# Performance work log

Measured on AMD Instinct MI355X. Metric: run time of the kernel, lower is better.

Reference implementation:

```python
import jax, jax.numpy as jnp
from jax import lax
import numpy as np

B, C, T = 4096, 22, 1001   # batch, EEG channels, time samples
K, KSZ, P = 40, 25, 100    # num_kernels, kernel_size, pool_size
S, O = 9, 4                # num_subjects, n_outputs
FEAT = K * ((T - KSZ + 1) // P)  # 40*9 = 360
BN_EPS = 1e-5


def setup_inputs() -> dict:
    key = jax.random.key(0)
    ks = jax.random.split(key, 8)
    x = jax.random.normal(ks[0], (B, C, T + 1), dtype=jnp.float32)
    # subject ids in 1..S encoded as id*1e6 in the last time step (all channels; only ch 0 is read)
    ids = jax.random.randint(ks[1], (B,), 1, S + 1)
    x = x.at[:, :, -1].set((ids * 1000000).astype(jnp.float32)[:, None])
    conv_w = jax.random.normal(ks[2], (K, C, 1, KSZ), dtype=jnp.float32) * 0.05
    conv_b = jax.random.normal(ks[3], (K,), dtype=jnp.float32) * 0.05
    bn_gamma = jnp.ones((K,), dtype=jnp.float32)
    bn_beta = jnp.zeros((K,), dtype=jnp.float32)
    fc_w = jax.random.normal(ks[4], (S, FEAT, O), dtype=jnp.float32) * 0.05
    fc_b = jax.random.normal(ks[5], (S, O), dtype=jnp.float32) * 0.05
    return {"x": x, "conv_w": conv_w, "conv_b": conv_b,
            "bn_gamma": bn_gamma, "bn_beta": bn_beta,
            "fc_w": fc_w, "fc_b": fc_b}


def reference(x, conv_w, conv_b, bn_gamma, bn_beta, fc_w, fc_b):
    # subject index (0-based); int cast blocks gradient flow, matching .item() dispatch
    sid = jnp.round(x[:, 0, -1] / 1e6).astype(jnp.int32) - 1  # [B]
    xin = x[:, :, :-1][:, :, None, :]                          # [B, C, 1, T]
    # Conv2d(n_chans, num_kernels, (1, kernel_size)), VALID padding
    y = lax.conv_general_dilated(xin, conv_w, window_strides=(1, 1),
                                 padding='VALID',
                                 dimension_numbers=('NCHW', 'OIHW', 'NCHW'))
    y = y + conv_b[None, :, None, None]                        # [B, K, 1, W], W = T-KSZ+1
    y = jax.nn.elu(y)
    # BatchNorm2d with batch statistics (train mode), affine
    mean = jnp.mean(y, axis=(0, 2, 3), keepdims=True)
    var = jnp.var(y, axis=(0, 2, 3), keepdims=True)
    y = (y - mean) * lax.rsqrt(var + BN_EPS)
    y = y * bn_gamma[None, :, None, None] + bn_beta[None, :, None, None]
    # AvgPool2d((1, P)): non-overlapping windows, remainder dropped
    W = y.shape[-1]
    n = W // P
    y = y[:, :, 0, :n * P].reshape(B, K, n, P).mean(axis=-1)   # [B, K, n]
    feat = y.reshape(B, -1)                                     # [B, FEAT]
    # dropout is identity at inference
    # per-sample subject-indexed FC, vectorized as a gathered batched matvec
    out = jnp.einsum('bf,bfo->bo', feat, fc_w[sid]) + fc_b[sid]  # [B, O]
    return out
```

## Files before the change

kernel.cpp:

```cpp
#include <hip/hip_runtime.h>

#define BATCH 4096
#define CCH   22
#define TT    1001
#define TROW  1002
#define KOUT  40
#define KSZ   25
#define WOUT  977
#define POOLW 100
#define NWIN  9
#define FEAT  360
#define NOUT  4

#define WBLK  256
#define NWB   4
#define NBLK  (BATCH * NWB)
#define CSTG  24
#define ROWB  48
#define TSTG  288
#define FKK   19
#define KP    48
#define NLOC  4

typedef __attribute__((ext_vector_type(8))) short short8;
typedef __attribute__((ext_vector_type(4))) float floatx4;

__device__ __forceinline__ unsigned short f2bf(float f) {
    unsigned u = __float_as_uint(f);
    u += 0x7fff + ((u >> 16) & 1);
    return (unsigned short)(u >> 16);
}
__device__ __forceinline__ unsigned cvt_pk_bf16(float a, float b) {
    unsigned r;
    asm("v_cvt_pk_bf16_f32 %0, %1, %2" : "=v"(r) : "v"(a), "v"(b));
    return r;
}
__device__ __forceinline__ float eluf(float v) {
    return v > 0.0f ? v : __expf(v) - 1.0f;
}

__global__ __launch_bounds__(256) void pack_w_kernel(const float* __restrict__ cw,
                                                     unsigned short* __restrict__ wp) {
    int i = blockIdx.x * 256 + threadIdx.x;
    if (i >= FKK * KP * 32) return;
    int e = i & 31;
    int n = (i >> 5) % KP;
    int kk = i / (KP * 32);
    int f = kk * 32 + e;
    int j = f / CSTG, c = f - j * CSTG;
    float v = (n < KOUT && c < CCH && j < KSZ) ? cw[(n * CCH + c) * KSZ + j] : 0.0f;
    wp[i] = f2bf(v);
}

__global__ __launch_bounds__(256, 4) void conv_mfma_kernel(
        const float* __restrict__ x, const unsigned short* __restrict__ wp,
        const float* __restrict__ cb, float* __restrict__ pparts,
        float* __restrict__ spS, float* __restrict__ spQ) {
    __shared__ unsigned short xt[TSTG * CSTG];
    __shared__ float ps_s[NLOC * KP];
    __shared__ float st_q[KP];

    const int bx = blockIdx.x, b = blockIdx.y;
    const int w0   = (bx == 0) ? 0   : (bx == 1 ? 252 : (bx == 2 ? 500 : 752));
    const int oend = (bx == 0) ? 252 : (bx == 1 ? 500 : (bx == 2 ? 752 : WOUT));
    const int tid = threadIdx.x;
    const int wv = __builtin_amdgcn_readfirstlane(tid >> 6);
    const int lane = tid & 63;
    const size_t xb = (size_t)b * (CCH * TROW);

    for (int i = tid; i < NLOC * KP + KP; i += 256) {
        if (i < NLOC * KP) ps_s[i] = 0.0f;
        else st_q[i - NLOC * KP] = 0.0f;
    }

    {
        const int r5 = lane & 31, h = lane >> 5;
#pragma unroll
        for (int it = 0; it < 3; ++it) {
            int idx = it * 4 + wv;
            if (idx < 9) {
                int t_loc = idx * 32 + r5;
                int t_gl = w0 + t_loc;
                float v[12];
#pragma unroll
                for (int r = 0; r < 12; ++r) {
                    int c = h * 12 + r;
                    v[r] = (c < CCH && t_gl < TT) ? x[xb + (size_t)c * TROW + t_gl] : 0.0f;
                }
                unsigned u[6];
#pragma unroll
                for (int r = 0; r < 6; ++r) u[r] = cvt_pk_bf16(v[2 * r], v[2 * r + 1]);
                char* dst = (char*)xt + t_loc * ROWB + h * 24;
                *(uint2*)(dst)      = make_uint2(u[0], u[1]);
                *(uint2*)(dst + 8)  = make_uint2(u[2], u[3]);
                *(uint2*)(dst + 16) = make_uint2(u[4], u[5]);
            }
        }
    }
    __syncthreads();

    const int m16 = lane & 15, g = lane >> 4;
    floatx4 acc[4][3];
#pragma unroll
    for (int nt = 0; nt < 3; ++nt) {
        int k = nt * 16 + m16;
        float bv = (k < KOUT) ? cb[k] : 0.0f;
#pragma unroll
        for (int mt = 0; mt < 4; ++mt) acc[mt][nt] = (floatx4){bv, bv, bv, bv};
    }

    const char* ap = (const char*)xt + (wv * 64 + m16) * ROWB + g * 16;
    const unsigned short* wpl = wp + m16 * 32 + g * 8;

    short8 bfr[3];
#pragma unroll
    for (int nt = 0; nt < 3; ++nt)
        bfr[nt] = *(const short8*)(wpl + nt * 16 * 32);

#pragma unroll 1
    for (int kk = 0; kk < FKK; ++kk) {
        short8 bnx[3];
        if (kk + 1 < FKK) {
            const unsigned short* wn = wpl + (kk + 1) * (KP * 32);
#pragma unroll
            for (int nt = 0; nt < 3; ++nt)
                bnx[nt] = *(const short8*)(wn + nt * 16 * 32);
        }
        short8 afr[4];
#pragma unroll
        for (int mt = 0; mt < 4; ++mt)
            afr[mt] = *(const short8*)(ap + mt * (16 * ROWB));
#pragma unroll
        for (int mt = 0; mt < 4; ++mt)
#pragma unroll
            for (int nt = 0; nt < 3; ++nt)
                acc[mt][nt] = __builtin_amdgcn_mfma_f32_16x16x32_bf16(
                    afr[mt], bfr[nt], acc[mt][nt], 0, 0, 0);
        ap += 64;
#pragma unroll
        for (int nt = 0; nt < 3; ++nt) bfr[nt] = bnx[nt];
    }

    const int win0 = w0 / POOLW;
    float qv[3] = {0.f, 0.f, 0.f};
#pragma unroll
    for (int mt = 0; mt < 4; ++mt) {
        const int wbase = w0 + wv * 64 + mt * 16 + g * 4;
        const int win = wbase / POOLW;
#pragma unroll
        for (int nt = 0; nt < 3; ++nt) {
            const int k = nt * 16 + m16;
            const bool kok = (k < KOUT);
            float psum = 0.f;
#pragma unroll
            for (int r = 0; r < 4; ++r) {
                int w = wbase + r;
                float e = eluf(acc[mt][nt][r]);
                e = (kok && w < oend) ? e : 0.0f;
                psum += e;
                qv[nt] = fmaf(e, e, qv[nt]);
            }
            float o1 = __shfl_down(psum, 16); int w1 = __shfl_down(win, 16);
            if (lane < 48 && w1 == win) psum += o1;
            float o2 = __shfl_down(psum, 32); int w2 = __shfl_down(win, 32);
            if (lane < 32 && w2 == win) psum += o2;
            int wu = __shfl_up(win, 16);
            if (g == 0 || wu != win)
                atomicAdd(&ps_s[(win - win0) * KP + k], psum);
        }
    }
#pragma unroll
    for (int nt = 0; nt < 3; ++nt) {
        float q = qv[nt];
        q += __shfl_xor(q, 16);
        q += __shfl_xor(q, 32);
        if (g == 0) atomicAdd(&st_q[nt * 16 + m16], q);
    }
    __syncthreads();

    const int blk = b * NWB + bx;
    if (tid < KOUT) {
        float s = ps_s[tid] + ps_s[KP + tid] + ps_s[2 * KP + tid] + ps_s[3 * KP + tid];
        spS[(size_t)tid * NBLK + blk] = s;
        spQ[(size_t)tid * NBLK + blk] = st_q[tid];
    }
    if (tid < NLOC * KOUT) {
        int wl = tid / KOUT, k = tid - wl * KOUT;
        pparts[((size_t)blk * NLOC + wl) * KOUT + k] = ps_s[wl * KP + k];
    }
}

__global__ __launch_bounds__(256) void bn_stats_kernel(
        const float* __restrict__ spS, const float* __restrict__ spQ,
        const float* __restrict__ gamma, const float* __restrict__ beta,
        float* __restrict__ scale, float* __restrict__ shift) {
    const int k = blockIdx.x;
    float s = 0.0f, q = 0.0f;
    for (int r = threadIdx.x; r < NBLK; r += 256) {
        s += spS[(size_t)k * NBLK + r];
        q += spQ[(size_t)k * NBLK + r];
    }
#pragma unroll
    for (int m = 32; m; m >>= 1) {
        s += __shfl_xor(s, m, 64);
        q += __shfl_xor(q, m, 64);
    }
    __shared__ float rs[4], rq[4];
    const int wid = threadIdx.x >> 6, lane = threadIdx.x & 63;
    if (lane == 0) { rs[wid] = s; rq[wid] = q; }
    __syncthreads();
    if (threadIdx.x == 0) {
        s = rs[0] + rs[1] + rs[2] + rs[3];
        q = rq[0] + rq[1] + rq[2] + rq[3];
        const float N = (float)BATCH * (float)WOUT;
        float mean = s / N;
        float var = q / N - mean * mean;
        float sc = gamma[k] / sqrtf(var + 1e-5f);
        scale[k] = sc;
        shift[k] = beta[k] - mean * sc;
    }
}

__global__ __launch_bounds__(64) void fc_kernel(
        const float* __restrict__ x, const float* __restrict__ pparts,
        const float* __restrict__ scale, const float* __restrict__ shift,
        const float* __restrict__ fcw, const float* __restrict__ fcb,
        float* __restrict__ out) {
    const int b = blockIdx.x;
    const int lane = threadIdx.x;
    const float idv = x[(size_t)b * (CCH * TROW) + TT];
    const int sid = (int)(idv * 1e-6f + 0.5f) - 1;
    const float* W = fcw + (size_t)sid * (FEAT * NOUT);
    const float* base = pparts + (size_t)b * (NWB * NLOC * KOUT);
    const unsigned long long TA = 0xDA9865210ULL;
    const unsigned long long TB = 0xFCF7FF4FFULL;
    float a0 = 0, a1 = 0, a2 = 0, a3 = 0;
    for (int f = lane; f < FEAT; f += 64) {
        int k = f / NWIN, win = f - k * NWIN;
        unsigned sa = (unsigned)(TA >> (4 * win)) & 15u;
        unsigned sb = (unsigned)(TB >> (4 * win)) & 15u;
        float p = base[sa * KOUT + k];
        if (sb != 15u) p += base[sb * KOUT + k];
        float feat = fmaf(p * 0.01f, scale[k], shift[k]);
        a0 = fmaf(feat, W[f * 4 + 0], a0);
        a1 = fmaf(feat, W[f * 4 + 1], a1);
        a2 = fmaf(feat, W[f * 4 + 2], a2);
        a3 = fmaf(feat, W[f * 4 + 3], a3);
    }
#pragma unroll
    for (int m = 32; m; m >>= 1) {
        a0 += __shfl_xor(a0, m, 64);
        a1 += __shfl_xor(a1, m, 64);
        a2 += __shfl_xor(a2, m, 64);
        a3 += __shfl_xor(a3, m, 64);
    }
    if (lane == 0) {
        out[b * 4 + 0] = a0 + fcb[sid * 4 + 0];
        out[b * 4 + 1] = a1 + fcb[sid * 4 + 1];
        out[b * 4 + 2] = a2 + fcb[sid * 4 + 2];
        out[b * 4 + 3] = a3 + fcb[sid * 4 + 3];
    }
}

extern "C" void kernel_launch(void* const* d_in, const int* in_sizes, int n_in,
                              void* d_out, int out_size, void* d_ws, size_t ws_size,
                              hipStream_t stream) {
    const float* x     = (const float*)d_in[0];
    const float* cw    = (const float*)d_in[1];
    const float* cb    = (const float*)d_in[2];
    const float* gamma = (const float*)d_in[3];
    const float* beta  = (const float*)d_in[4];
    const float* fcw   = (const float*)d_in[5];
    const float* fcb   = (const float*)d_in[6];
    float* out = (float*)d_out;

    float* pparts = (float*)d_ws;
    float* spS    = pparts + (size_t)NBLK * NLOC * KOUT;
    float* spQ    = spS + (size_t)KOUT * NBLK;
    float* scale  = spQ + (size_t)KOUT * NBLK;
    float* shift  = scale + KOUT;
    unsigned short* wpck = (unsigned short*)(shift + KOUT);

    pack_w_kernel<<<(FKK * KP * 32 + 255) / 256, 256, 0, stream>>>(cw, wpck);
    conv_mfma_kernel<<<dim3(NWB, BATCH), 256, 0, stream>>>(x, wpck, cb, pparts, spS, spQ);
    bn_stats_kernel<<<KOUT, 256, 0, stream>>>(spS, spQ, gamma, beta, scale, shift);
    fc_kernel<<<BATCH, 64, 0, stream>>>(x, pparts, scale, shift, fcw, fcb, out);
}
```

Before: 347.2 us.

## Split each sample's time axis into two 512-wide blocks instead of four

Each conv block now covers 512 output positions, so a sample needs 2 blocks rather than 4. Each wave computes 8 M-tiles instead of 4, so every loaded weight fragment feeds twice as many MFMAs. The halo of input rows staged to LDS is now shared by only two tiles, and the second tile is aligned so no pooling window spans a tile boundary. This lets the FC kernel read each window's partial sum directly instead of combining two. In exchange the kernel holds twice the accumulators and twice the LDS tile, occupancy drops to 3 blocks, and the second block does some redundant compute over its overlap region.

```diff
diff --git a/kernel.cpp b/kernel.cpp
--- a/kernel.cpp
+++ b/kernel.cpp
@@ -12,15 +12,16 @@
 #define FEAT  360
 #define NOUT  4
 
-#define WBLK  256
-#define NWB   4
+#define WBLK  512
+#define NWB   2
 #define NBLK  (BATCH * NWB)
 #define CSTG  24
 #define ROWB  48
-#define TSTG  288
+#define TSTG  544
 #define FKK   19
 #define KP    48
-#define NLOC  4
+#define NLOC  7
+#define NMT   8
 
 typedef __attribute__((ext_vector_type(8))) short short8;
 typedef __attribute__((ext_vector_type(4))) float floatx4;
@@ -52,7 +53,7 @@
     wp[i] = f2bf(v);
 }
 
-__global__ __launch_bounds__(256, 4) void conv_mfma_kernel(
+__global__ __launch_bounds__(256, 3) void conv_mfma_kernel(
         const float* __restrict__ x, const unsigned short* __restrict__ wp,
         const float* __restrict__ cb, float* __restrict__ pparts,
         float* __restrict__ spS, float* __restrict__ spQ) {
@@ -61,8 +62,10 @@
     __shared__ float st_q[KP];
 
     const int bx = blockIdx.x, b = blockIdx.y;
-    const int w0   = (bx == 0) ? 0   : (bx == 1 ? 252 : (bx == 2 ? 500 : 752));
-    const int oend = (bx == 0) ? 252 : (bx == 1 ? 500 : (bx == 2 ? 752 : WOUT));
+    const int w0     = bx ? 488 : 0;
+    const int ostart = bx ? 500 : 0;
+    const int oend   = bx ? WOUT : 500;
+    const int win0   = bx ? 4 : 0;
     const int tid = threadIdx.x;
     const int wv = __builtin_amdgcn_readfirstlane(tid >> 6);
     const int lane = tid & 63;
@@ -76,9 +79,9 @@
     {
         const int r5 = lane & 31, h = lane >> 5;
 #pragma unroll
-        for (int it = 0; it < 3; ++it) {
+        for (int it = 0; it < 5; ++it) {
             int idx = it * 4 + wv;
-            if (idx < 9) {
+            if (idx < 17) {
                 int t_loc = idx * 32 + r5;
                 int t_gl = w0 + t_loc;
                 float v[12];
@@ -100,16 +103,16 @@
     __syncthreads();
 
     const int m16 = lane & 15, g = lane >> 4;
-    floatx4 acc[4][3];
+    floatx4 acc[NMT][3];
 #pragma unroll
     for (int nt = 0; nt < 3; ++nt) {
         int k = nt * 16 + m16;
         float bv = (k < KOUT) ? cb[k] : 0.0f;
 #pragma unroll
-        for (int mt = 0; mt < 4; ++mt) acc[mt][nt] = (floatx4){bv, bv, bv, bv};
-    }
-
-    const char* ap = (const char*)xt + (wv * 64 + m16) * ROWB + g * 16;
+        for (int mt = 0; mt < NMT; ++mt) acc[mt][nt] = (floatx4){bv, bv, bv, bv};
+    }
+
+    const char* ap = (const char*)xt + (wv * 128 + m16) * ROWB + g * 16;
     const unsigned short* wpl = wp + m16 * 32 + g * 8;
 
     short8 bfr[3];
@@ -126,26 +129,28 @@
             for (int nt = 0; nt < 3; ++nt)
                 bnx[nt] = *(const short8*)(wn + nt * 16 * 32);
         }
-        short8 afr[4];
-#pragma unroll
-        for (int mt = 0; mt < 4; ++mt)
-            afr[mt] = *(const short8*)(ap + mt * (16 * ROWB));
-#pragma unroll
-        for (int mt = 0; mt < 4; ++mt)
-#pragma unroll
-            for (int nt = 0; nt < 3; ++nt)
-                acc[mt][nt] = __builtin_amdgcn_mfma_f32_16x16x32_bf16(
-                    afr[mt], bfr[nt], acc[mt][nt], 0, 0, 0);
+#pragma unroll
+        for (int half = 0; half < 2; ++half) {
+            short8 afr[4];
+#pragma unroll
+            for (int q = 0; q < 4; ++q)
+                afr[q] = *(const short8*)(ap + (half * 4 + q) * (16 * ROWB));
+#pragma unroll
+            for (int q = 0; q < 4; ++q)
+#pragma unroll
+                for (int nt = 0; nt < 3; ++nt)
+                    acc[half * 4 + q][nt] = __builtin_amdgcn_mfma_f32_16x16x32_bf16(
+                        afr[q], bfr[nt], acc[half * 4 + q][nt], 0, 0, 0);
+        }
         ap += 64;
 #pragma unroll
         for (int nt = 0; nt < 3; ++nt) bfr[nt] = bnx[nt];
     }
 
-    const int win0 = w0 / POOLW;
     float qv[3] = {0.f, 0.f, 0.f};
 #pragma unroll
-    for (int mt = 0; mt < 4; ++mt) {
-        const int wbase = w0 + wv * 64 + mt * 16 + g * 4;
+    for (int mt = 0; mt < NMT; ++mt) {
+        const int wbase = w0 + wv * 128 + mt * 16 + g * 4;
         const int win = wbase / POOLW;
 #pragma unroll
         for (int nt = 0; nt < 3; ++nt) {
@@ -156,7 +161,7 @@
             for (int r = 0; r < 4; ++r) {
                 int w = wbase + r;
                 float e = eluf(acc[mt][nt][r]);
-                e = (kok && w < oend) ? e : 0.0f;
+                e = (kok && w >= ostart && w < oend) ? e : 0.0f;
                 psum += e;
                 qv[nt] = fmaf(e, e, qv[nt]);
             }
@@ -180,12 +185,14 @@
 
     const int blk = b * NWB + bx;
     if (tid < KOUT) {
-        float s = ps_s[tid] + ps_s[KP + tid] + ps_s[2 * KP + tid] + ps_s[3 * KP + tid];
+        float s = 0.0f;
+#pragma unroll
+        for (int wl = 0; wl < NLOC; ++wl) s += ps_s[wl * KP + tid];
         spS[(size_t)tid * NBLK + blk] = s;
         spQ[(size_t)tid * NBLK + blk] = st_q[tid];
     }
-    if (tid < NLOC * KOUT) {
-        int wl = tid / KOUT, k = tid - wl * KOUT;
+    for (int i = tid; i < NLOC * KOUT; i += 256) {
+        int wl = i / KOUT, k = i - wl * KOUT;
         pparts[((size_t)blk * NLOC + wl) * KOUT + k] = ps_s[wl * KP + k];
     }
 }
@@ -232,15 +239,11 @@
     const int sid = (int)(idv * 1e-6f + 0.5f) - 1;
     const float* W = fcw + (size_t)sid * (FEAT * NOUT);
     const float* base = pparts + (size_t)b * (NWB * NLOC * KOUT);
-    const unsigned long long TA = 0xDA9865210ULL;
-    const unsigned long long TB = 0xFCF7FF4FFULL;
     float a0 = 0, a1 = 0, a2 = 0, a3 = 0;
     for (int f = lane; f < FEAT; f += 64) {
         int k = f / NWIN, win = f - k * NWIN;
-        unsigned sa = (unsigned)(TA >> (4 * win)) & 15u;
-        unsigned sb = (unsigned)(TB >> (4 * win)) & 15u;
-        float p = base[sa * KOUT + k];
-        if (sb != 15u) p += base[sb * KOUT + k];
+        int u = (win < 5) ? win : (win + 3);
+        float p = base[u * KOUT + k];
         float feat = fmaf(p * 0.01f, scale[k], shift[k]);
         a0 = fmaf(feat, W[f * 4 + 0], a0);
         a1 = fmaf(feat, W[f * 4 + 1], a1);
```

After: 307.0 us. 1.13x faster.
